# Optimization experiments

Measured on AMD Instinct MI355X. Metric: run time of the kernel, lower is better.

## Reference

```python
import jax, jax.numpy as jnp
import numpy as np

# YOLOv1 config constants
GRIDS = 7
CLASSES = 20
IMAGE_SIZE = 448.0
LAMBDA_COOR = 5.0
LAMBDA_NOOBJ = 0.5
FEAT = 5 + CLASSES  # 25


def _make_target(bboxes):
    """bboxes: (B, n, 5) pixel coords [x1,y1,x2,y2,label] -> target (B,G,G,25).
    First-write-wins per grid cell, matching the torch per-box loop."""
    B, n, _ = bboxes.shape
    box = bboxes[..., :4] / IMAGE_SIZE                      # (B,n,4) in [0,1]
    label = bboxes[..., 4].astype(jnp.int32)                # (B,n)
    xc = (box[..., 0] + box[..., 2]) * 0.5
    yc = (box[..., 1] + box[..., 3]) * 0.5
    w = box[..., 2] - box[..., 0]
    h = box[..., 3] - box[..., 1]
    xg = jnp.floor(xc * GRIDS).astype(jnp.int32)
    yg = jnp.floor(yc * GRIDS).astype(jnp.int32)
    xo = xc * GRIDS - xg
    yo = yc * GRIDS - yg
    cell = yg * GRIDS + xg                                  # (B,n) flat cell id
    # first-come-first-serve: drop box j if an earlier box k<j hit the same cell
    same = cell[:, :, None] == cell[:, None, :]             # (B,n,n)
    earlier = jnp.tril(jnp.ones((n, n), dtype=bool), k=-1)
    keep = ~jnp.any(same & earlier, axis=-1)                # (B,n)
    one_hot = jax.nn.one_hot(label, CLASSES, dtype=jnp.float32)
    vals = jnp.concatenate(
        [xo[..., None], yo[..., None], w[..., None], h[..., None],
         jnp.ones_like(xo)[..., None], one_hot], axis=-1)   # (B,n,25)
    # route dropped boxes to an out-of-range index -> scatter drops them;
    # kept boxes have unique cells per image so .set is deterministic
    flat_idx = jnp.arange(B, dtype=jnp.int32)[:, None] * (GRIDS * GRIDS) + cell
    flat_idx = jnp.where(keep, flat_idx, B * GRIDS * GRIDS)  # OOB sentinel
    target = jnp.zeros((B * GRIDS * GRIDS, FEAT), dtype=jnp.float32)
    target = target.at[flat_idx.reshape(-1)].set(
        vals.reshape(-1, FEAT), mode='drop')
    return target.reshape(B, GRIDS, GRIDS, FEAT)


def reference(pred, bboxes):
    target = _make_target(bboxes)
    obj_mask = target[:, :, :, 4]
    noobj_mask = (1.0 - obj_mask) * LAMBDA_NOOBJ
    loss_contain = (target[:, :, :, 4] - pred[:, :, :, 4]) ** 2
    loss_contain = ((obj_mask + noobj_mask) * loss_contain).sum((1, 2))
    loss_coord = ((target[:, :, :, 0] - pred[:, :, :, 0]) ** 2
                  + (target[:, :, :, 1] - pred[:, :, :, 1]) ** 2
                  + (jnp.sqrt(target[:, :, :, 2]) - jnp.sqrt(pred[:, :, :, 2])) ** 2
                  + (jnp.sqrt(target[:, :, :, 3]) - jnp.sqrt(pred[:, :, :, 3])) ** 2)
    loss_coord = (obj_mask * loss_coord * LAMBDA_COOR).sum((1, 2))
    loss_class = (target[:, :, :, 5:] - pred[:, :, :, 5:]) ** 2
    loss_class = (obj_mask[..., None] * loss_class).sum((1, 2, 3))
    return (loss_contain + loss_coord + loss_class).mean()


def setup_inputs() -> dict:
    key = jax.random.key(0)
    k1, k2, k3, k4, k5 = jax.random.split(key, 5)
    B, n = 16384, 8
    # pred in (0.05, 0.95) so sqrt of w/h channels is well-defined
    pred = jax.random.uniform(k1, (B, GRIDS, GRIDS, FEAT), dtype=jnp.float32) * 0.9 + 0.05
    # valid boxes in pixels: centers in (0.25,0.75)*448, sizes in (0.05,0.4)*448
    cx = (jax.random.uniform(k2, (B, n)) * 0.5 + 0.25) * IMAGE_SIZE
    cy = (jax.random.uniform(k3, (B, n)) * 0.5 + 0.25) * IMAGE_SIZE
    wh = (jax.random.uniform(k4, (B, n, 2)) * 0.35 + 0.05) * IMAGE_SIZE
    x1 = cx - wh[..., 0] * 0.5
    x2 = cx + wh[..., 0] * 0.5
    y1 = cy - wh[..., 1] * 0.5
    y2 = cy + wh[..., 1] * 0.5
    label = jax.random.randint(k5, (B, n), 0, CLASSES).astype(jnp.float32)
    bboxes = jnp.stack([x1, y1, x2, y2, label], axis=-1).astype(jnp.float32)
    return {"pred": pred, "bboxes": bboxes}
```

## Files before the change

### kernel.cpp

```cpp
#include <hip/hip_runtime.h>

#define GRIDS 7
#define NCELL 49
#define NFEAT 25
#define CELLSZ 1225
#define BPB 16
#define MAXBOX 16


__device__ __forceinline__ float conf_of(float4 v, unsigned e0) {
    unsigned q = (e0 * 5243u) >> 17;
    unsigned r = e0 - q * 25u;
    return (r == 4u) ? v.x : (r == 3u) ? v.y : (r == 2u) ? v.z
         : (r == 1u) ? v.w : 0.f;
}

__global__ __launch_bounds__(256) void yolo_main(
    const float* __restrict__ pred, const float* __restrict__ bbox,
    float* __restrict__ partial, int B, int nbox)
{
    __shared__ float sBox[BPB * MAXBOX * 5];
    __shared__ int   sOff[BPB * MAXBOX];
    __shared__ int   sKeep[BPB * MAXBOX];
    __shared__ float sRed[4];

    const int tid = threadIdx.x;
    const long long b0 = (long long)blockIdx.x * BPB;
    const int nb = min(BPB, B - (int)b0);
    const int nbx = nb * nbox;
    const int nelem = nb * CELLSZ;
    const int nvec  = nelem >> 2;
    const float* pb = pred + b0 * CELLSZ;
    const float4* p4 = (const float4*)pb;

    float4 pf0 = make_float4(0.f, 0.f, 0.f, 0.f), pf1 = pf0, pf2 = pf0, pf3 = pf0;
    if (tid       < nvec) pf0 = p4[tid];
    if (tid + 256 < nvec) pf1 = p4[tid + 256];
    if (tid + 512 < nvec) pf2 = p4[tid + 512];
    if (tid + 768 < nvec) pf3 = p4[tid + 768];

    if (tid < nbx) {
        const float* bx = bbox + (b0 * nbox + tid) * 5;
        float x1 = bx[0] / 448.f, y1 = bx[1] / 448.f;
        float x2 = bx[2] / 448.f, y2 = bx[3] / 448.f;
        float xc = (x1 + x2) * 0.5f, yc = (y1 + y2) * 0.5f;
        float w  = x2 - x1,          h  = y2 - y1;
        float xs = xc * (float)GRIDS, ys = yc * (float)GRIDS;
        float xg = floorf(xs), yg = floorf(ys);
        int lb = tid / nbox;
        int cell = (int)yg * GRIDS + (int)xg;
        sOff[tid] = lb * CELLSZ + cell * NFEAT;
        float* e = &sBox[tid * 5];
        e[0] = xs - xg; e[1] = ys - yg;
        e[2] = sqrtf(w); e[3] = sqrtf(h);
        e[4] = bx[4];
    }
    __syncthreads();

    if (tid < nbx) {
        int lb = tid / nbox;
        int o  = sOff[tid];
        int k = 1;
        for (int j = lb * nbox; j < tid; ++j)
            if (sOff[j] == o) { k = 0; break; }
        sKeep[tid] = k;
    }
    __syncthreads();

    const int wid = tid >> 6, lane = tid & 63;
    const int f = lane & 31;
    const int cbase = wid * 2 + (lane >> 5);
    float gv[16];
    #pragma unroll
    for (int k = 0; k < 16; ++k) {
        int bi = cbase + 8 * k;
        bool v = (bi < nbx) && (f < NFEAT) && sKeep[bi];
        gv[k] = v ? pb[sOff[bi] + f] : 0.f;
    }

    float acc = 0.f;
    if (tid       < nvec) { float c = conf_of(pf0, (unsigned)tid << 2);         acc = fmaf(0.5f * c, c, acc); }
    if (tid + 256 < nvec) { float c = conf_of(pf1, (unsigned)(tid + 256) << 2); acc = fmaf(0.5f * c, c, acc); }
    if (tid + 512 < nvec) { float c = conf_of(pf2, (unsigned)(tid + 512) << 2); acc = fmaf(0.5f * c, c, acc); }
    if (tid + 768 < nvec) { float c = conf_of(pf3, (unsigned)(tid + 768) << 2); acc = fmaf(0.5f * c, c, acc); }

    int i = tid + 1024;
    for (; i + 768 < nvec; i += 1024) {
        float4 a = p4[i];
        float4 b = p4[i + 256];
        float4 c = p4[i + 512];
        float4 d = p4[i + 768];
        float ca = conf_of(a, (unsigned)i << 2);
        float cb = conf_of(b, (unsigned)(i + 256) << 2);
        float cc = conf_of(c, (unsigned)(i + 512) << 2);
        float cd = conf_of(d, (unsigned)(i + 768) << 2);
        acc = fmaf(0.5f * ca, ca, acc);
        acc = fmaf(0.5f * cb, cb, acc);
        acc = fmaf(0.5f * cc, cc, acc);
        acc = fmaf(0.5f * cd, cd, acc);
    }
    for (; i < nvec; i += 256) {
        float4 a = p4[i];
        float c = conf_of(a, (unsigned)i << 2);
        acc = fmaf(0.5f * c, c, acc);
    }
    for (int e = (nvec << 2) + tid; e < nelem; e += 256) {
        unsigned q = ((unsigned)e * 5243u) >> 17;
        if ((unsigned)e - q * 25u == 4u) {
            float p = pb[e];
            acc = fmaf(0.5f * p, p, acc);
        }
    }

    #pragma unroll
    for (int k = 0; k < 16; ++k) {
        int bi = cbase + 8 * k;
        bool v = (bi < nbx) && (f < NFEAT) && sKeep[bi];
        if (v) {
            const float* e = &sBox[bi * 5];
            float p = gv[k];
            float term;
            if (f == 4) {
                float d = 1.f - p;
                term = fmaf(d, d, -0.5f * p * p);
            } else if (f < 4) {
                float q = (f >= 2) ? sqrtf(p) : p;
                float d = e[f] - q;
                term = 5.f * d * d;
            } else {
                float t = ((int)e[4] == f - 5) ? 1.f : 0.f;
                float d = t - p;
                term = d * d;
            }
            acc += term;
        }
    }

    for (int off = 32; off; off >>= 1)
        acc += __shfl_down(acc, off, 64);
    if ((tid & 63) == 0) sRed[tid >> 6] = acc;
    __syncthreads();
    if (tid == 0)
        partial[blockIdx.x] = sRed[0] + sRed[1] + sRed[2] + sRed[3];
}

__global__ __launch_bounds__(256) void yolo_reduce(
    const float* __restrict__ partial, int n, float* __restrict__ out, int B)
{
    __shared__ double s[256];
    const float4* p4 = (const float4*)partial;
    const int n4 = n >> 2;
    double a = 0.0;
    for (int j = threadIdx.x; j < n4; j += 256) {
        float4 v = p4[j];
        a += (double)v.x + (double)v.y + (double)v.z + (double)v.w;
    }
    for (int j = (n4 << 2) + threadIdx.x; j < n; j += 256)
        a += (double)partial[j];
    s[threadIdx.x] = a;
    __syncthreads();
    for (int str = 128; str; str >>= 1) {
        if (threadIdx.x < str) s[threadIdx.x] += s[threadIdx.x + str];
        __syncthreads();
    }
    if (threadIdx.x == 0) out[0] = (float)(s[0] / (double)B);
}

extern "C" void kernel_launch(void* const* d_in, const int* in_sizes, int n_in,
                              void* d_out, int out_size, void* d_ws, size_t ws_size,
                              hipStream_t stream) {
    const float* pred = (const float*)d_in[0];
    const float* bbox = (const float*)d_in[1];
    int B = in_sizes[0] / CELLSZ;
    int nbox = in_sizes[1] / (B * 5);
    if (nbox > MAXBOX) nbox = MAXBOX;
    float* out = (float*)d_out;
    float* partial = (float*)d_ws;

    int nblocks = (B + BPB - 1) / BPB;
    yolo_main<<<nblocks, 256, 0, stream>>>(pred, bbox, partial, B, nbox);
    yolo_reduce<<<1, 256, 0, stream>>>(partial, nblocks, out, B);
}
```

Baseline: 27.23 us.

## Fuse final reduction into main kernel via fixed-point atomics and last-block finish

Removes the separate single-block reduce kernel. Each block now atomically adds its partial sum, converted to 64-bit fixed point, into a global accumulator and bumps a counter, and the last block to arrive writes the final mean. This saves one kernel launch and the serial tail reduction, but adds a memset launch and 1024 atomics. Fixed-point scaling gives deterministic summation but limits precision and range.

```diff
diff --git a/kernel.cpp b/kernel.cpp
--- a/kernel.cpp
+++ b/kernel.cpp
@@ -6,6 +6,7 @@
 #define CELLSZ 1225
 #define BPB 16
 #define MAXBOX 16
+#define FIXSCALE 1048576.0
 
 
 __device__ __forceinline__ float conf_of(float4 v, unsigned e0) {
@@ -15,9 +16,10 @@
          : (r == 1u) ? v.w : 0.f;
 }
 
-__global__ __launch_bounds__(256) void yolo_main(
+__global__ __launch_bounds__(256) void yolo_fused(
     const float* __restrict__ pred, const float* __restrict__ bbox,
-    float* __restrict__ partial, int B, int nbox)
+    unsigned long long* __restrict__ acc64, unsigned* __restrict__ counter,
+    float* __restrict__ out, int B, int nbox, int nblocks)
 {
     __shared__ float sBox[BPB * MAXBOX * 5];
     __shared__ int   sOff[BPB * MAXBOX];
@@ -140,30 +142,23 @@
         acc += __shfl_down(acc, off, 64);
     if ((tid & 63) == 0) sRed[tid >> 6] = acc;
     __syncthreads();
-    if (tid == 0)
-        partial[blockIdx.x] = sRed[0] + sRed[1] + sRed[2] + sRed[3];
-}
 
-__global__ __launch_bounds__(256) void yolo_reduce(
-    const float* __restrict__ partial, int n, float* __restrict__ out, int B)
-{
-    __shared__ double s[256];
-    const float4* p4 = (const float4*)partial;
-    const int n4 = n >> 2;
-    double a = 0.0;
-    for (int j = threadIdx.x; j < n4; j += 256) {
-        float4 v = p4[j];
-        a += (double)v.x + (double)v.y + (double)v.z + (double)v.w;
+    if (tid == 0) {
+        float bsum = sRed[0] + sRed[1] + sRed[2] + sRed[3];
+        unsigned long long fx =
+            (unsigned long long)__double2ll_rn((double)bsum * FIXSCALE);
+        __hip_atomic_fetch_add(acc64, fx, __ATOMIC_RELAXED,
+                               __HIP_MEMORY_SCOPE_AGENT);
+        asm volatile("s_waitcnt vmcnt(0)" ::: "memory");
+        unsigned prev = __hip_atomic_fetch_add(counter, 1u, __ATOMIC_RELAXED,
+                                               __HIP_MEMORY_SCOPE_AGENT);
+        if (prev == (unsigned)(nblocks - 1)) {
+            unsigned long long tot =
+                __hip_atomic_load(acc64, __ATOMIC_RELAXED,
+                                  __HIP_MEMORY_SCOPE_AGENT);
+            out[0] = (float)(((double)(long long)tot / FIXSCALE) / (double)B);
+        }
     }
-    for (int j = (n4 << 2) + threadIdx.x; j < n; j += 256)
-        a += (double)partial[j];
-    s[threadIdx.x] = a;
-    __syncthreads();
-    for (int str = 128; str; str >>= 1) {
-        if (threadIdx.x < str) s[threadIdx.x] += s[threadIdx.x + str];
-        __syncthreads();
-    }
-    if (threadIdx.x == 0) out[0] = (float)(s[0] / (double)B);
 }
 
 extern "C" void kernel_launch(void* const* d_in, const int* in_sizes, int n_in,
@@ -175,9 +170,12 @@
     int nbox = in_sizes[1] / (B * 5);
     if (nbox > MAXBOX) nbox = MAXBOX;
     float* out = (float*)d_out;
-    float* partial = (float*)d_ws;
+
+    unsigned long long* acc64 = (unsigned long long*)d_ws;
+    unsigned* counter = (unsigned*)((char*)d_ws + 64);
 
     int nblocks = (B + BPB - 1) / BPB;
-    yolo_main<<<nblocks, 256, 0, stream>>>(pred, bbox, partial, B, nbox);
-    yolo_reduce<<<1, 256, 0, stream>>>(partial, nblocks, out, B);
+    hipMemsetAsync(d_ws, 0, 128, stream);
+    yolo_fused<<<nblocks, 256, 0, stream>>>(pred, bbox, acc64, counter, out,
+                                            B, nbox, nblocks);
 }
```

New measurement: 45.42 us. 66.8% more time.
